# Kernel tuning notes

Hardware: AMD Instinct MI355X
Metric: run time of the kernel (lower is better)

Reference implementation:

```python
import jax, jax.numpy as jnp
import numpy as np

N, E = 50000, 800000
F_N, F_E = 32, 16
HC, H, C, L = 128, 2, 64, 3  # hidden_channels, heads, out per head, num_layers
NEG_SLOPE = 0.2  # PyG GATConv default


def setup_inputs() -> dict:
    key = jax.random.key(0)
    ks = jax.random.split(key, 32)
    rn = lambda k, shape, s=0.05: (jax.random.normal(k, shape, jnp.float32) * s)
    return {
        "x": jax.random.normal(ks[0], (N, F_N), jnp.float32),
        "edge_index": jax.random.randint(ks[1], (2, E), 0, N),
        "edge_attr": jax.random.normal(ks[2], (E, F_E), jnp.float32),
        # node encoder: Linear(32,128) -> ReLU -> Linear(128,128)
        "w_n1": rn(ks[3], (F_N, HC)), "b_n1": jnp.zeros((HC,), jnp.float32),
        "w_n2": rn(ks[4], (HC, HC)), "b_n2": jnp.zeros((HC,), jnp.float32),
        # edge encoder: Linear(16,128) -> ReLU (output is ignored by GATConv, edge_dim=None)
        "w_e": rn(ks[5], (F_E, HC)), "b_e": jnp.zeros((HC,), jnp.float32),
        # 3 GATConv layers: lin [128,H*C], att_src/att_dst [H,C], bias [H*C]
        "conv_w": rn(ks[6], (L, HC, H * C)),
        "conv_att_src": rn(ks[7], (L, H, C)),
        "conv_att_dst": rn(ks[8], (L, H, C)),
        "conv_b": jnp.zeros((L, H * C), jnp.float32),
        # path prediction head: Linear(256,128)->ReLU->Linear(128,64)->ReLU->Linear(64,1)->Sigmoid
        "wp1": rn(ks[9], (2 * HC, HC)), "bp1": jnp.zeros((HC,), jnp.float32),
        "wp2": rn(ks[10], (HC, 64)), "bp2": jnp.zeros((64,), jnp.float32),
        "wp3": rn(ks[11], (64, 1)), "bp3": jnp.zeros((1,), jnp.float32),
        # vulnerability head: Linear(128,64)->ReLU->Linear(64,1)->Sigmoid
        "wv1": rn(ks[12], (HC, 64)), "bv1": jnp.zeros((64,), jnp.float32),
        "wv2": rn(ks[13], (64, 1)), "bv2": jnp.zeros((1,), jnp.float32),
    }


def _gat_layer(x, src, dst, w, att_src, att_dst, bias):
    n = x.shape[0]
    h = (x @ w).reshape(n, H, C)                       # [N,H,C]
    a_src = jnp.sum(h * att_src, axis=-1)              # [N,H]
    a_dst = jnp.sum(h * att_dst, axis=-1)              # [N,H]
    alpha = a_src[src] + a_dst[dst]                    # [E',H]
    alpha = jax.nn.leaky_relu(alpha, NEG_SLOPE)
    amax = jax.lax.stop_gradient(jax.ops.segment_max(alpha, dst, num_segments=n))
    ex = jnp.exp(alpha - amax[dst])
    denom = jax.ops.segment_sum(ex, dst, num_segments=n)  # [N,H] (>0: self-loops)
    coef = ex / denom[dst]                             # softmax over incoming edges
    msg = h[src] * coef[:, :, None]                    # [E',H,C]
    out = jax.ops.segment_sum(msg, dst, num_segments=n)
    return out.reshape(n, H * C) + bias


def reference(x, edge_index, edge_attr,
              w_n1, b_n1, w_n2, b_n2, w_e, b_e,
              conv_w, conv_att_src, conv_att_dst, conv_b,
              wp1, bp1, wp2, bp2, wp3, bp3, wv1, bv1, wv2, bv2):
    n = x.shape[0]
    # node encoder (dropout = identity in eval)
    h = jax.nn.relu(x @ w_n1 + b_n1) @ w_n2 + b_n2
    # edge encoder output is computed but ignored by GATConv (edge_dim=None in PyG)
    _edge_emb = jax.nn.relu(edge_attr @ w_e + b_e)
    # add self loops (GATConv default add_self_loops=True)
    loop = jnp.arange(n, dtype=edge_index.dtype)
    src = jnp.concatenate([edge_index[0], loop])
    dst = jnp.concatenate([edge_index[1], loop])
    for l in range(L):
        h = jax.nn.relu(_gat_layer(h, src, dst, conv_w[l], conv_att_src[l], conv_att_dst[l], conv_b[l]))
    g = jnp.mean(h, axis=0, keepdims=True)             # [1,128] graph embedding
    # path head on cat(x[:1], graph_embedding)
    p = jnp.concatenate([h[:1], g], axis=1)            # [1,256]
    p = jax.nn.relu(p @ wp1 + bp1)
    p = jax.nn.relu(p @ wp2 + bp2)
    path = jax.nn.sigmoid(p @ wp3 + bp3)               # [1,1]
    v = jax.nn.relu(h @ wv1 + bv1)
    vuln = jax.nn.sigmoid(v @ wv2 + bv2)               # [N,1]
    esc = jnp.zeros((1, 1), jnp.float32)               # [1,1]
    return (path, vuln, esc)
```

## Files before the change

kernel.cpp:

```cpp
#include <hip/hip_runtime.h>
#include <math.h>

#define HC 128
#define NSLOPE 0.2f

__device__ __forceinline__ float lrelu(float v){ return v > 0.f ? v : NSLOPE * v; }

__device__ __forceinline__ unsigned short f2bf(float f){
    unsigned int b = __float_as_uint(f);
    b += 0x7FFFu + ((b >> 16) & 1u);
    return (unsigned short)(b >> 16);
}
__device__ __forceinline__ float bf_lo(unsigned int v){ return __uint_as_float(v << 16); }
__device__ __forceinline__ float bf_hi(unsigned int v){ return __uint_as_float(v & 0xFFFF0000u); }
__device__ __forceinline__ float bf1(unsigned short v){ return __uint_as_float((unsigned int)v << 16); }

__global__ void count_kernel(const int* __restrict__ ei, int* __restrict__ cnt,
                             int* __restrict__ rank, int E){
    int e = blockIdx.x * blockDim.x + threadIdx.x;
    if (e < E) rank[e] = atomicAdd(&cnt[ei[E + e]], 1);
}

__global__ __launch_bounds__(256) void scan_part_kernel(
        const int* __restrict__ deg, int* __restrict__ bsum, int n)
{
    int t = threadIdx.x, lane = t & 63, wid = t >> 6;
    int base = blockIdx.x * 1024 + t * 4;
    int s = 0;
    #pragma unroll
    for (int j = 0; j < 4; ++j){ int i = base + j; if (i < n) s += deg[i]; }
    #pragma unroll
    for (int o = 1; o < 64; o <<= 1) s += __shfl_xor(s, o);
    __shared__ int red[4];
    if (lane == 0) red[wid] = s;
    __syncthreads();
    if (t == 0) bsum[blockIdx.x] = red[0] + red[1] + red[2] + red[3];
}

__global__ __launch_bounds__(64) void scan_top_kernel(
        const int* __restrict__ bsum, int* __restrict__ boff, int* __restrict__ rowptr,
        int nb, int n)
{
    int t = threadIdx.x;
    int v = (t < nb) ? bsum[t] : 0;
    int incl = v;
    #pragma unroll
    for (int o = 1; o < 64; o <<= 1){ int u = __shfl_up(incl, o); if (t >= o) incl += u; }
    if (t < nb) boff[t] = incl - v;
    if (t == 63) rowptr[n] = incl;
}

__global__ __launch_bounds__(256) void scan_fin_kernel(
        const int* __restrict__ deg, const int* __restrict__ boff,
        int* __restrict__ rowptr, int n)
{
    int t = threadIdx.x, lane = t & 63, wid = t >> 6;
    int base = blockIdx.x * 1024 + t * 4;
    int d[4]; int s = 0;
    #pragma unroll
    for (int j = 0; j < 4; ++j){ int i = base + j; d[j] = (i < n) ? deg[i] : 0; s += d[j]; }
    int incl = s;
    #pragma unroll
    for (int o = 1; o < 64; o <<= 1){ int u = __shfl_up(incl, o); if (lane >= o) incl += u; }
    __shared__ int wsum[4];
    if (lane == 63) wsum[wid] = incl;
    __syncthreads();
    int off = boff[blockIdx.x] + (incl - s);
    for (int w = 0; w < wid; ++w) off += wsum[w];
    #pragma unroll
    for (int j = 0; j < 4; ++j){
        int i = base + j;
        if (i < n) rowptr[i] = off;
        off += d[j];
    }
}

__global__ __launch_bounds__(256) void scatter_kernel(
        const int* __restrict__ ei, const int* __restrict__ rowptr,
        const int* __restrict__ rank, int* __restrict__ colsrc, int E)
{
    int b = blockIdx.x * 1024 + threadIdx.x;
    int e0 = b, e1 = b + 256, e2 = b + 512, e3 = b + 768;
    bool v0 = e0 < E, v1 = e1 < E, v2 = e2 < E, v3 = e3 < E;
    int d0=0,d1=0,d2=0,d3=0, s0=0,s1=0,s2=0,s3=0, r0=0,r1=0,r2=0,r3=0;
    if (v0){ d0 = ei[E + e0]; s0 = ei[e0]; r0 = rank[e0]; }
    if (v1){ d1 = ei[E + e1]; s1 = ei[e1]; r1 = rank[e1]; }
    if (v2){ d2 = ei[E + e2]; s2 = ei[e2]; r2 = rank[e2]; }
    if (v3){ d3 = ei[E + e3]; s3 = ei[e3]; r3 = rank[e3]; }
    if (v0) colsrc[rowptr[d0] + r0] = s0;
    if (v1) colsrc[rowptr[d1] + r1] = s1;
    if (v2) colsrc[rowptr[d2] + r2] = s2;
    if (v3) colsrc[rowptr[d3] + r3] = s3;
}

__global__ __launch_bounds__(256) void enc1_kernel(
        const float* __restrict__ x, const float* __restrict__ w1, const float* __restrict__ b1,
        unsigned short* __restrict__ hid, int n)
{
    __shared__ float As[32][68];
    __shared__ float Bs[32][128];
    int t = threadIdx.x;
    int m0 = blockIdx.x * 64;
    int tm = t >> 4, tn = t & 15;

    #pragma unroll
    for (int i = 0; i < 2; ++i){
        int f = i * 256 + t;
        int row = f >> 3, kq = f & 7;
        int gr = m0 + row; if (gr > n - 1) gr = n - 1;
        float4 v = *(const float4*)(x + (size_t)gr * 32 + kq * 4);
        As[kq*4+0][row] = v.x; As[kq*4+1][row] = v.y; As[kq*4+2][row] = v.z; As[kq*4+3][row] = v.w;
    }
    #pragma unroll
    for (int i = 0; i < 4; ++i){
        int f = i * 256 + t;
        int kk = f >> 5, nq = f & 31;
        *(float4*)&Bs[kk][nq*4] = *(const float4*)(w1 + (size_t)kk * 128 + nq * 4);
    }
    __syncthreads();

    float acc[4][8];
    #pragma unroll
    for (int i = 0; i < 4; ++i)
        #pragma unroll
        for (int j = 0; j < 8; ++j) acc[i][j] = 0.f;

    #pragma unroll 4
    for (int k = 0; k < 32; ++k){
        float a[4], b[8];
        *(float4*)&a[0] = *(float4*)&As[k][tm*4];
        *(float4*)&b[0] = *(float4*)&Bs[k][tn*8];
        *(float4*)&b[4] = *(float4*)&Bs[k][tn*8+4];
        #pragma unroll
        for (int i = 0; i < 4; ++i)
            #pragma unroll
            for (int j = 0; j < 8; ++j) acc[i][j] = fmaf(a[i], b[j], acc[i][j]);
    }

    float bb[8];
    *(float4*)&bb[0] = *(const float4*)(b1 + tn*8);
    *(float4*)&bb[4] = *(const float4*)(b1 + tn*8 + 4);
    #pragma unroll
    for (int i = 0; i < 4; ++i){
        int node = m0 + tm*4 + i;
        if (node < n){
            float o[8];
            #pragma unroll
            for (int j = 0; j < 8; ++j) o[j] = fmaxf(acc[i][j] + bb[j], 0.f);
            uint4 pk;
            pk.x = (unsigned int)f2bf(o[0]) | ((unsigned int)f2bf(o[1]) << 16);
            pk.y = (unsigned int)f2bf(o[2]) | ((unsigned int)f2bf(o[3]) << 16);
            pk.z = (unsigned int)f2bf(o[4]) | ((unsigned int)f2bf(o[5]) << 16);
            pk.w = (unsigned int)f2bf(o[6]) | ((unsigned int)f2bf(o[7]) << 16);
            *(uint4*)(hid + (size_t)node*HC + tn*8) = pk;
        }
    }
}

template<bool ATT>
__global__ __launch_bounds__(256) void gemm_main_kernel(
        const unsigned short* __restrict__ A, const float* __restrict__ W, const float* __restrict__ bias,
        const float* __restrict__ att_s, const float* __restrict__ att_d,
        unsigned short* __restrict__ Cb,
        float* __restrict__ asrc, float* __restrict__ adst, int n)
{
    __shared__ float As[32][68];
    __shared__ float Bs[32][128];
    int t = threadIdx.x;
    int m0 = blockIdx.x * 64;
    int tm = t >> 4, tn = t & 15;

    float acc[4][8];
    #pragma unroll
    for (int i = 0; i < 4; ++i)
        #pragma unroll
        for (int j = 0; j < 8; ++j) acc[i][j] = 0.f;

    for (int kc = 0; kc < 4; ++kc){
        int k0 = kc * 32;
        {
            int row = t >> 2, kq = t & 3;
            int gr = m0 + row; if (gr > n - 1) gr = n - 1;
            uint4 v = *(const uint4*)(A + (size_t)gr * HC + k0 + kq * 8);
            As[kq*8+0][row] = bf_lo(v.x); As[kq*8+1][row] = bf_hi(v.x);
            As[kq*8+2][row] = bf_lo(v.y); As[kq*8+3][row] = bf_hi(v.y);
            As[kq*8+4][row] = bf_lo(v.z); As[kq*8+5][row] = bf_hi(v.z);
            As[kq*8+6][row] = bf_lo(v.w); As[kq*8+7][row] = bf_hi(v.w);
        }
        #pragma unroll
        for (int i = 0; i < 4; ++i){
            int f = i * 256 + t;
            int kk = f >> 5, nq = f & 31;
            *(float4*)&Bs[kk][nq*4] = *(const float4*)(W + (size_t)(k0 + kk) * 128 + nq * 4);
        }
        __syncthreads();
        #pragma unroll 4
        for (int k = 0; k < 32; ++k){
            float a[4], b[8];
            *(float4*)&a[0] = *(float4*)&As[k][tm*4];
            *(float4*)&b[0] = *(float4*)&Bs[k][tn*8];
            *(float4*)&b[4] = *(float4*)&Bs[k][tn*8+4];
            #pragma unroll
            for (int i = 0; i < 4; ++i)
                #pragma unroll
                for (int j = 0; j < 8; ++j) acc[i][j] = fmaf(a[i], b[j], acc[i][j]);
        }
        __syncthreads();
    }

    float bb[8];
    if (!ATT){
        *(float4*)&bb[0] = *(const float4*)(bias + tn*8);
        *(float4*)&bb[4] = *(const float4*)(bias + tn*8 + 4);
    } else {
        #pragma unroll
        for (int j = 0; j < 8; ++j) bb[j] = 0.f;
    }
    #pragma unroll
    for (int i = 0; i < 4; ++i){
        int node = m0 + tm*4 + i;
        if (node < n){
            float o[8];
            #pragma unroll
            for (int j = 0; j < 8; ++j) o[j] = acc[i][j] + bb[j];
            uint4 pk;
            pk.x = (unsigned int)f2bf(o[0]) | ((unsigned int)f2bf(o[1]) << 16);
            pk.y = (unsigned int)f2bf(o[2]) | ((unsigned int)f2bf(o[3]) << 16);
            pk.z = (unsigned int)f2bf(o[4]) | ((unsigned int)f2bf(o[5]) << 16);
            pk.w = (unsigned int)f2bf(o[6]) | ((unsigned int)f2bf(o[7]) << 16);
            *(uint4*)(Cb + (size_t)node*HC + tn*8) = pk;
        }
    }

    if (ATT){
        float ats[8], atd[8];
        *(float4*)&ats[0] = *(const float4*)(att_s + tn*8);
        *(float4*)&ats[4] = *(const float4*)(att_s + tn*8 + 4);
        *(float4*)&atd[0] = *(const float4*)(att_d + tn*8);
        *(float4*)&atd[4] = *(const float4*)(att_d + tn*8 + 4);
        #pragma unroll
        for (int i = 0; i < 4; ++i){
            float sa = 0.f, sd = 0.f;
            #pragma unroll
            for (int j = 0; j < 8; ++j){
                sa = fmaf(acc[i][j], ats[j], sa);
                sd = fmaf(acc[i][j], atd[j], sd);
            }
            sa += __shfl_xor(sa, 1); sa += __shfl_xor(sa, 2); sa += __shfl_xor(sa, 4);
            sd += __shfl_xor(sd, 1); sd += __shfl_xor(sd, 2); sd += __shfl_xor(sd, 4);
            int node = m0 + tm*4 + i;
            if ((tn == 0 || tn == 8) && node < n){
                int head = tn >> 3;
                asrc[(size_t)node*2 + head] = sa;
                adst[(size_t)node*2 + head] = sd;
            }
        }
    }
}

__global__ __launch_bounds__(64) void aggregate_kernel(
        const unsigned short* __restrict__ h1b, const float* __restrict__ asrc, const float* __restrict__ adst,
        const int* __restrict__ rowptr, const int* __restrict__ colsrc,
        const float* __restrict__ bias, unsigned short* __restrict__ hout, int n)
{
    __shared__ float4 exl[64];
    int i = blockIdx.x;
    if (i >= n) return;
    int t = threadIdx.x;
    int head = t >> 5;
    float2 adv = *(const float2*)(adst + (size_t)i * 2);
    float2 asv = *(const float2*)(asrc + (size_t)i * 2);
    float ads = head ? adv.y : adv.x;
    float exs = __expf(lrelu((head ? asv.y : asv.x) + ads));
    unsigned int hv = ((const unsigned int*)(h1b + (size_t)i * HC))[t];
    float acc0 = exs * bf_lo(hv), acc1 = exs * bf_hi(hv), D = exs;

    int e  = rowptr[i];
    int e1 = rowptr[i + 1];
    while (e < e1){
        int m = e1 - e; if (m > 64) m = 64;
        if (t < m){
            int s = colsrc[e + t];
            float2 as = *(const float2*)(asrc + (size_t)s * 2);
            exl[t] = make_float4(__int_as_float(s),
                                 __expf(lrelu(as.x + adv.x)),
                                 __expf(lrelu(as.y + adv.y)), 0.f);
        }
        __syncthreads();
        int j = 0;
        for (; j + 4 <= m; j += 4){
            float4 q0 = exl[j], q1 = exl[j+1], q2 = exl[j+2], q3 = exl[j+3];
            const unsigned int* p0 = (const unsigned int*)(h1b + (size_t)__float_as_int(q0.x) * HC);
            const unsigned int* p1 = (const unsigned int*)(h1b + (size_t)__float_as_int(q1.x) * HC);
            const unsigned int* p2 = (const unsigned int*)(h1b + (size_t)__float_as_int(q2.x) * HC);
            const unsigned int* p3 = (const unsigned int*)(h1b + (size_t)__float_as_int(q3.x) * HC);
            unsigned int v0 = p0[t], v1 = p1[t], v2 = p2[t], v3 = p3[t];
            float c0 = head ? q0.z : q0.y;
            float c1 = head ? q1.z : q1.y;
            float c2 = head ? q2.z : q2.y;
            float c3 = head ? q3.z : q3.y;
            acc0 = fmaf(c0, bf_lo(v0), acc0);  acc1 = fmaf(c0, bf_hi(v0), acc1);
            acc0 = fmaf(c1, bf_lo(v1), acc0);  acc1 = fmaf(c1, bf_hi(v1), acc1);
            acc0 = fmaf(c2, bf_lo(v2), acc0);  acc1 = fmaf(c2, bf_hi(v2), acc1);
            acc0 = fmaf(c3, bf_lo(v3), acc0);  acc1 = fmaf(c3, bf_hi(v3), acc1);
            D += (c0 + c1) + (c2 + c3);
        }
        for (; j < m; ++j){
            float4 q = exl[j];
            unsigned int v = ((const unsigned int*)(h1b + (size_t)__float_as_int(q.x) * HC))[t];
            float c = head ? q.z : q.y;
            acc0 = fmaf(c, bf_lo(v), acc0);
            acc1 = fmaf(c, bf_hi(v), acc1);
            D += c;
        }
        __syncthreads();
        e += m;
    }
    float rD = 1.0f / D;
    float o0 = fmaxf(acc0 * rD + bias[2*t],     0.f);
    float o1 = fmaxf(acc1 * rD + bias[2*t + 1], 0.f);
    ((unsigned int*)hout)[(size_t)i * 64 + t] =
        (unsigned int)f2bf(o0) | ((unsigned int)f2bf(o1) << 16);
}

__global__ __launch_bounds__(256) void mean_part_kernel(
        const unsigned short* __restrict__ h, float* __restrict__ partial, int n)
{
    int t = threadIdx.x;
    int cq = t & 31;
    int rl = t >> 5;
    float4 acc = make_float4(0.f, 0.f, 0.f, 0.f);
    for (int i = blockIdx.x * 8 + rl; i < n; i += gridDim.x * 8){
        uint2 v = *(const uint2*)(h + (size_t)i * HC + cq * 4);
        acc.x += bf_lo(v.x); acc.y += bf_hi(v.x);
        acc.z += bf_lo(v.y); acc.w += bf_hi(v.y);
    }
    __shared__ float4 red[256];
    red[t] = acc;
    __syncthreads();
    if (t < 128){
        float4 o = red[t + 128];
        red[t].x += o.x; red[t].y += o.y; red[t].z += o.z; red[t].w += o.w;
    }
    __syncthreads();
    if (t < 64){
        float4 o = red[t + 64];
        red[t].x += o.x; red[t].y += o.y; red[t].z += o.z; red[t].w += o.w;
    }
    __syncthreads();
    if (t < 32){
        float4 a = red[t], b = red[t + 32];
        float4 s = make_float4(a.x + b.x, a.y + b.y, a.z + b.z, a.w + b.w);
        *(float4*)(partial + (size_t)blockIdx.x * HC + t * 4) = s;
    }
}

__global__ __launch_bounds__(256) void mean_fin_kernel(
        const float* __restrict__ partial, float* __restrict__ g, int nb)
{
    int t = threadIdx.x;
    int cq = t & 31, b0 = t >> 5;
    float4 acc = make_float4(0.f, 0.f, 0.f, 0.f);
    for (int b = b0; b < nb; b += 8){
        float4 v = *(const float4*)(partial + (size_t)b * HC + cq * 4);
        acc.x += v.x; acc.y += v.y; acc.z += v.z; acc.w += v.w;
    }
    __shared__ float4 red[256];
    red[t] = acc;
    __syncthreads();
    if (t < 128){
        float4 o = red[t + 128];
        red[t].x += o.x; red[t].y += o.y; red[t].z += o.z; red[t].w += o.w;
    }
    __syncthreads();
    if (t < 64){
        float4 o = red[t + 64];
        red[t].x += o.x; red[t].y += o.y; red[t].z += o.z; red[t].w += o.w;
    }
    __syncthreads();
    if (t < 32){
        float4 a = red[t], b = red[t + 32];
        float4 s = make_float4(a.x + b.x, a.y + b.y, a.z + b.z, a.w + b.w);
        *(float4*)(g + t * 4) = s;
    }
}

__global__ __launch_bounds__(256) void vuln_fused_kernel(
        const unsigned short* __restrict__ h, const float* __restrict__ wv1, const float* __restrict__ bv1,
        const float* __restrict__ wv2, const float* __restrict__ bv2,
        float* __restrict__ out, int n)
{
    __shared__ float As[32][68];
    __shared__ float Bs[32][64];
    int t = threadIdx.x;
    int m0 = blockIdx.x * 64;
    int tm = t >> 4, tn = t & 15;

    float acc[4][4];
    #pragma unroll
    for (int i = 0; i < 4; ++i)
        #pragma unroll
        for (int j = 0; j < 4; ++j) acc[i][j] = 0.f;

    for (int kc = 0; kc < 4; ++kc){
        int k0 = kc * 32;
        {
            int row = t >> 2, kq = t & 3;
            int gr = m0 + row; if (gr > n - 1) gr = n - 1;
            uint4 v = *(const uint4*)(h + (size_t)gr * HC + k0 + kq * 8);
            As[kq*8+0][row] = bf_lo(v.x); As[kq*8+1][row] = bf_hi(v.x);
            As[kq*8+2][row] = bf_lo(v.y); As[kq*8+3][row] = bf_hi(v.y);
            As[kq*8+4][row] = bf_lo(v.z); As[kq*8+5][row] = bf_hi(v.z);
            As[kq*8+6][row] = bf_lo(v.w); As[kq*8+7][row] = bf_hi(v.w);
        }
        #pragma unroll
        for (int i = 0; i < 2; ++i){
            int f = i * 256 + t;
            int kk = f >> 4, nq = f & 15;
            *(float4*)&Bs[kk][nq*4] = *(const float4*)(wv1 + (size_t)(k0 + kk) * 64 + nq * 4);
        }
        __syncthreads();
        #pragma unroll 4
        for (int k = 0; k < 32; ++k){
            float a[4], b[4];
            *(float4*)&a[0] = *(float4*)&As[k][tm*4];
            *(float4*)&b[0] = *(float4*)&Bs[k][tn*4];
            #pragma unroll
            for (int i = 0; i < 4; ++i)
                #pragma unroll
                for (int j = 0; j < 4; ++j) acc[i][j] = fmaf(a[i], b[j], acc[i][j]);
        }
        __syncthreads();
    }

    float bb[4], wv[4];
    *(float4*)&bb[0] = *(const float4*)(bv1 + tn*4);
    *(float4*)&wv[0] = *(const float4*)(wv2 + tn*4);
    float bv2v = bv2[0];
    #pragma unroll
    for (int i = 0; i < 4; ++i){
        float v = 0.f;
        #pragma unroll
        for (int j = 0; j < 4; ++j) v = fmaf(fmaxf(acc[i][j] + bb[j], 0.f), wv[j], v);
        v += __shfl_xor(v, 1); v += __shfl_xor(v, 2);
        v += __shfl_xor(v, 4); v += __shfl_xor(v, 8);
        int node = m0 + tm*4 + i;
        if (tn == 0 && node < n)
            out[1 + node] = 1.0f / (1.0f + __expf(-(v + bv2v)));
    }
}

__global__ __launch_bounds__(128) void path_kernel(
        const unsigned short* __restrict__ h, const float* __restrict__ g,
        const float* __restrict__ wp1, const float* __restrict__ bp1,
        const float* __restrict__ wp2, const float* __restrict__ bp2,
        const float* __restrict__ wp3, const float* __restrict__ bp3,
        float* __restrict__ out, int n)
{
    __shared__ float pc[256];
    __shared__ float p1[HC];
    __shared__ float p2[64];
    int t = threadIdx.x;
    pc[t]       = bf1(h[t]);
    pc[128 + t] = g[t] * (1.0f / (float)n);
    __syncthreads();
    float a = bp1[t];
    for (int k = 0; k < 256; ++k) a = fmaf(pc[k], wp1[k * HC + t], a);
    p1[t] = fmaxf(a, 0.f);
    __syncthreads();
    if (t < 64){
        float a2 = bp2[t];
        for (int k = 0; k < HC; ++k) a2 = fmaf(p1[k], wp2[k * 64 + t], a2);
        p2[t] = fmaxf(a2, 0.f);
    }
    __syncthreads();
    if (t == 0){
        float a3 = bp3[0];
        for (int k = 0; k < 64; ++k) a3 = fmaf(p2[k], wp3[k], a3);
        out[0] = 1.0f / (1.0f + __expf(-a3));
        out[1 + n] = 0.f;
    }
}

extern "C" void kernel_launch(void* const* d_in, const int* in_sizes, int n_in,
                              void* d_out, int out_size, void* d_ws, size_t ws_size,
                              hipStream_t stream)
{
    const float* x    = (const float*)d_in[0];
    const int*   ei   = (const int*)d_in[1];
    const float* w_n1 = (const float*)d_in[3];
    const float* b_n1 = (const float*)d_in[4];
    const float* w_n2 = (const float*)d_in[5];
    const float* b_n2 = (const float*)d_in[6];
    const float* conv_w = (const float*)d_in[9];
    const float* att_s  = (const float*)d_in[10];
    const float* att_d  = (const float*)d_in[11];
    const float* conv_b = (const float*)d_in[12];
    const float* wp1 = (const float*)d_in[13];
    const float* bp1 = (const float*)d_in[14];
    const float* wp2 = (const float*)d_in[15];
    const float* bp2 = (const float*)d_in[16];
    const float* wp3 = (const float*)d_in[17];
    const float* bp3 = (const float*)d_in[18];
    const float* wv1 = (const float*)d_in[19];
    const float* bv1 = (const float*)d_in[20];
    const float* wv2 = (const float*)d_in[21];
    const float* bv2 = (const float*)d_in[22];

    const int N = in_sizes[0] / 32;
    const int E = in_sizes[1] / 2;
    float* out = (float*)d_out;

    char* ws = (char*)d_ws;
    size_t off = 0;
    auto take = [&](size_t bytes) -> char* {
        char* p = ws + off;
        off += (bytes + 255) & ~(size_t)255;
        return p;
    };
    unsigned short* hA = (unsigned short*)take((size_t)N * HC * 2);
    unsigned short* hB = (unsigned short*)take((size_t)N * HC * 2);
    float* asrc  = (float*)take((size_t)N * 2 * 4);
    float* adst  = (float*)take((size_t)N * 2 * 4);
    int*   rowptr= (int*)take((size_t)(N + 1) * 4);
    int*   cnt   = (int*)take((size_t)N * 4);
    int*   rank  = (int*)take((size_t)E * 4);
    int*   colsrc= (int*)take((size_t)E * 4);
    float* g     = (float*)take(HC * 4);
    const int MB = 64;
    float* mpart = (float*)take((size_t)MB * HC * 4);
    int nb = (N + 1023) / 1024;
    int*   bsum  = (int*)take((size_t)((nb + 63) & ~63) * 4);
    int*   boff  = (int*)take((size_t)((nb + 63) & ~63) * 4);

    hipMemsetAsync(cnt, 0, (size_t)N * 4, stream);
    count_kernel<<<(E + 255) / 256, 256, 0, stream>>>(ei, cnt, rank, E);
    scan_part_kernel<<<nb, 256, 0, stream>>>(cnt, bsum, N);
    scan_top_kernel<<<1, 64, 0, stream>>>(bsum, boff, rowptr, nb, N);
    scan_fin_kernel<<<nb, 256, 0, stream>>>(cnt, boff, rowptr, N);
    scatter_kernel<<<(E + 1023) / 1024, 256, 0, stream>>>(ei, rowptr, rank, colsrc, E);

    int nblk64 = (N + 63) / 64;
    enc1_kernel<<<nblk64, 256, 0, stream>>>(x, w_n1, b_n1, hB, N);
    gemm_main_kernel<false><<<nblk64, 256, 0, stream>>>(
        hB, w_n2, b_n2, nullptr, nullptr, hA, nullptr, nullptr, N);

    for (int l = 0; l < 3; ++l){
        gemm_main_kernel<true><<<nblk64, 256, 0, stream>>>(
            hA, conv_w + (size_t)l * HC * HC, nullptr,
            att_s + (size_t)l * HC, att_d + (size_t)l * HC,
            hB, asrc, adst, N);
        aggregate_kernel<<<N, 64, 0, stream>>>(
            hB, asrc, adst, rowptr, colsrc, conv_b + (size_t)l * HC, hA, N);
    }

    mean_part_kernel<<<MB, 256, 0, stream>>>(hA, mpart, N);
    mean_fin_kernel<<<1, 256, 0, stream>>>(mpart, g, MB);
    vuln_fused_kernel<<<nblk64, 256, 0, stream>>>(hA, wv1, bv1, wv2, bv2, out, N);
    path_kernel<<<1, 128, 0, stream>>>(hA, g, wp1, bp1, wp2, bp2, wp3, bp3, out, N);
}
```

Before: 372.5 us.

## Split GEMM over column halves and move attention dots to separate kernel

The main GEMM now runs twice as many blocks, each covering 64 output columns with a 4x4 per-thread tile and a smaller shared B tile, which should raise occupancy and parallelism. The attention-score dot products, which needed the full 128 columns in one block, move into a new att_kernel that rereads the bf16 projected features. The A-tile load mapping also changes so that consecutive threads cover consecutive rows (LDS write pattern), in both the main and vulnerability GEMMs. The cost is an extra launch per layer and an extra read of the projected features. Attention now uses bf16-rounded values rather than fp32 accumulators, a small precision change.

```diff
diff --git a/kernel.cpp b/kernel.cpp
--- a/kernel.cpp
+++ b/kernel.cpp
@@ -157,104 +157,101 @@
     }
 }
 
-template<bool ATT>
 __global__ __launch_bounds__(256) void gemm_main_kernel(
-        const unsigned short* __restrict__ A, const float* __restrict__ W, const float* __restrict__ bias,
-        const float* __restrict__ att_s, const float* __restrict__ att_d,
-        unsigned short* __restrict__ Cb,
-        float* __restrict__ asrc, float* __restrict__ adst, int n)
+        const unsigned short* __restrict__ A, const float* __restrict__ W,
+        const float* __restrict__ bias, unsigned short* __restrict__ Cb, int n)
 {
     __shared__ float As[32][68];
-    __shared__ float Bs[32][128];
-    int t = threadIdx.x;
-    int m0 = blockIdx.x * 64;
+    __shared__ float Bs[32][68];
+    int t = threadIdx.x;
+    int m0 = (blockIdx.x >> 1) * 64;
+    int c0 = (blockIdx.x & 1) * 64;
     int tm = t >> 4, tn = t & 15;
-
-    float acc[4][8];
+    int kq = t >> 6, arow = t & 63;
+
+    float acc[4][4];
     #pragma unroll
     for (int i = 0; i < 4; ++i)
         #pragma unroll
-        for (int j = 0; j < 8; ++j) acc[i][j] = 0.f;
+        for (int j = 0; j < 4; ++j) acc[i][j] = 0.f;
 
     for (int kc = 0; kc < 4; ++kc){
         int k0 = kc * 32;
         {
-            int row = t >> 2, kq = t & 3;
-            int gr = m0 + row; if (gr > n - 1) gr = n - 1;
+            int gr = m0 + arow; if (gr > n - 1) gr = n - 1;
             uint4 v = *(const uint4*)(A + (size_t)gr * HC + k0 + kq * 8);
-            As[kq*8+0][row] = bf_lo(v.x); As[kq*8+1][row] = bf_hi(v.x);
-            As[kq*8+2][row] = bf_lo(v.y); As[kq*8+3][row] = bf_hi(v.y);
-            As[kq*8+4][row] = bf_lo(v.z); As[kq*8+5][row] = bf_hi(v.z);
-            As[kq*8+6][row] = bf_lo(v.w); As[kq*8+7][row] = bf_hi(v.w);
-        }
-        #pragma unroll
-        for (int i = 0; i < 4; ++i){
+            As[kq*8+0][arow] = bf_lo(v.x); As[kq*8+1][arow] = bf_hi(v.x);
+            As[kq*8+2][arow] = bf_lo(v.y); As[kq*8+3][arow] = bf_hi(v.y);
+            As[kq*8+4][arow] = bf_lo(v.z); As[kq*8+5][arow] = bf_hi(v.z);
+            As[kq*8+6][arow] = bf_lo(v.w); As[kq*8+7][arow] = bf_hi(v.w);
+        }
+        #pragma unroll
+        for (int i = 0; i < 2; ++i){
             int f = i * 256 + t;
-            int kk = f >> 5, nq = f & 31;
-            *(float4*)&Bs[kk][nq*4] = *(const float4*)(W + (size_t)(k0 + kk) * 128 + nq * 4);
+            int kk = f >> 4, nq = f & 15;
+            *(float4*)&Bs[kk][nq*4] = *(const float4*)(W + (size_t)(k0 + kk) * 128 + c0 + nq * 4);
         }
         __syncthreads();
         #pragma unroll 4
         for (int k = 0; k < 32; ++k){
-            float a[4], b[8];
+            float a[4], b[4];
             *(float4*)&a[0] = *(float4*)&As[k][tm*4];
-            *(float4*)&b[0] = *(float4*)&Bs[k][tn*8];
-            *(float4*)&b[4] = *(float4*)&Bs[k][tn*8+4];
+            *(float4*)&b[0] = *(float4*)&Bs[k][tn*4];
             #pragma unroll
             for (int i = 0; i < 4; ++i)
                 #pragma unroll
-                for (int j = 0; j < 8; ++j) acc[i][j] = fmaf(a[i], b[j], acc[i][j]);
+                for (int j = 0; j < 4; ++j) acc[i][j] = fmaf(a[i], b[j], acc[i][j]);
         }
         __syncthreads();
     }
 
-    float bb[8];
-    if (!ATT){
-        *(float4*)&bb[0] = *(const float4*)(bias + tn*8);
-        *(float4*)&bb[4] = *(const float4*)(bias + tn*8 + 4);
+    float bb[4];
+    if (bias){
+        *(float4*)&bb[0] = *(const float4*)(bias + c0 + tn*4);
     } else {
         #pragma unroll
-        for (int j = 0; j < 8; ++j) bb[j] = 0.f;
+        for (int j = 0; j < 4; ++j) bb[j] = 0.f;
     }
     #pragma unroll
     for (int i = 0; i < 4; ++i){
         int node = m0 + tm*4 + i;
         if (node < n){
-            float o[8];
+            float o[4];
             #pragma unroll
-            for (int j = 0; j < 8; ++j) o[j] = acc[i][j] + bb[j];
-            uint4 pk;
+            for (int j = 0; j < 4; ++j) o[j] = acc[i][j] + bb[j];
+            uint2 pk;
             pk.x = (unsigned int)f2bf(o[0]) | ((unsigned int)f2bf(o[1]) << 16);
             pk.y = (unsigned int)f2bf(o[2]) | ((unsigned int)f2bf(o[3]) << 16);
-            pk.z = (unsigned int)f2bf(o[4]) | ((unsigned int)f2bf(o[5]) << 16);
-            pk.w = (unsigned int)f2bf(o[6]) | ((unsigned int)f2bf(o[7]) << 16);
-            *(uint4*)(Cb + (size_t)node*HC + tn*8) = pk;
-        }
-    }
-
-    if (ATT){
-        float ats[8], atd[8];
-        *(float4*)&ats[0] = *(const float4*)(att_s + tn*8);
-        *(float4*)&ats[4] = *(const float4*)(att_s + tn*8 + 4);
-        *(float4*)&atd[0] = *(const float4*)(att_d + tn*8);
-        *(float4*)&atd[4] = *(const float4*)(att_d + tn*8 + 4);
-        #pragma unroll
-        for (int i = 0; i < 4; ++i){
-            float sa = 0.f, sd = 0.f;
-            #pragma unroll
-            for (int j = 0; j < 8; ++j){
-                sa = fmaf(acc[i][j], ats[j], sa);
-                sd = fmaf(acc[i][j], atd[j], sd);
-            }
-            sa += __shfl_xor(sa, 1); sa += __shfl_xor(sa, 2); sa += __shfl_xor(sa, 4);
-            sd += __shfl_xor(sd, 1); sd += __shfl_xor(sd, 2); sd += __shfl_xor(sd, 4);
-            int node = m0 + tm*4 + i;
-            if ((tn == 0 || tn == 8) && node < n){
-                int head = tn >> 3;
-                asrc[(size_t)node*2 + head] = sa;
-                adst[(size_t)node*2 + head] = sd;
-            }
-        }
+            *(uint2*)(Cb + (size_t)node*HC + c0 + tn*4) = pk;
+        }
+    }
+}
+
+__global__ __launch_bounds__(256) void att_kernel(
+        const unsigned short* __restrict__ h1, const float* __restrict__ att_s,
+        const float* __restrict__ att_d, float* __restrict__ asrc, float* __restrict__ adst, int n)
+{
+    int t = threadIdx.x;
+    int node = blockIdx.x * 32 + (t >> 3);
+    int l8 = t & 7;
+    if (node >= n) return;
+    uint4 v0 = *(const uint4*)(h1 + (size_t)node * HC + l8 * 16);
+    uint4 v1 = *(const uint4*)(h1 + (size_t)node * HC + l8 * 16 + 8);
+    float sa = 0.f, sd = 0.f;
+    unsigned int w[8] = {v0.x, v0.y, v0.z, v0.w, v1.x, v1.y, v1.z, v1.w};
+    #pragma unroll
+    for (int q = 0; q < 8; ++q){
+        float lo = bf_lo(w[q]), hi = bf_hi(w[q]);
+        int c = l8 * 16 + q * 2;
+        sa = fmaf(lo, att_s[c], sa);     sa = fmaf(hi, att_s[c + 1], sa);
+        sd = fmaf(lo, att_d[c], sd);     sd = fmaf(hi, att_d[c + 1], sd);
+    }
+    sa += __shfl_xor(sa, 1); sa += __shfl_xor(sa, 2);
+    sd += __shfl_xor(sd, 1); sd += __shfl_xor(sd, 2);
+    if ((l8 & 3) == 0){
+        int head = l8 >> 2;
+        asrc[(size_t)node * 2 + head] = sa;
+        adst[(size_t)node * 2 + head] = sd;
     }
 }
 
@@ -395,6 +392,7 @@
     int t = threadIdx.x;
     int m0 = blockIdx.x * 64;
     int tm = t >> 4, tn = t & 15;
+    int kq = t >> 6, arow = t & 63;
 
     float acc[4][4];
     #pragma unroll
@@ -405,13 +403,12 @@
     for (int kc = 0; kc < 4; ++kc){
         int k0 = kc * 32;
         {
-            int row = t >> 2, kq = t & 3;
-            int gr = m0 + row; if (gr > n - 1) gr = n - 1;
+            int gr = m0 + arow; if (gr > n - 1) gr = n - 1;
             uint4 v = *(const uint4*)(h + (size_t)gr * HC + k0 + kq * 8);
-            As[kq*8+0][row] = bf_lo(v.x); As[kq*8+1][row] = bf_hi(v.x);
-            As[kq*8+2][row] = bf_lo(v.y); As[kq*8+3][row] = bf_hi(v.y);
-            As[kq*8+4][row] = bf_lo(v.z); As[kq*8+5][row] = bf_hi(v.z);
-            As[kq*8+6][row] = bf_lo(v.w); As[kq*8+7][row] = bf_hi(v.w);
+            As[kq*8+0][arow] = bf_lo(v.x); As[kq*8+1][arow] = bf_hi(v.x);
+            As[kq*8+2][arow] = bf_lo(v.y); As[kq*8+3][arow] = bf_hi(v.y);
+            As[kq*8+4][arow] = bf_lo(v.z); As[kq*8+5][arow] = bf_hi(v.z);
+            As[kq*8+6][arow] = bf_lo(v.w); As[kq*8+7][arow] = bf_hi(v.w);
         }
         #pragma unroll
         for (int i = 0; i < 2; ++i){
@@ -541,15 +538,15 @@
     scatter_kernel<<<(E + 1023) / 1024, 256, 0, stream>>>(ei, rowptr, rank, colsrc, E);
 
     int nblk64 = (N + 63) / 64;
+    int gemm_grid = nblk64 * 2;
     enc1_kernel<<<nblk64, 256, 0, stream>>>(x, w_n1, b_n1, hB, N);
-    gemm_main_kernel<false><<<nblk64, 256, 0, stream>>>(
-        hB, w_n2, b_n2, nullptr, nullptr, hA, nullptr, nullptr, N);
+    gemm_main_kernel<<<gemm_grid, 256, 0, stream>>>(hB, w_n2, b_n2, hA, N);
 
     for (int l = 0; l < 3; ++l){
-        gemm_main_kernel<true><<<nblk64, 256, 0, stream>>>(
-            hA, conv_w + (size_t)l * HC * HC, nullptr,
-            att_s + (size_t)l * HC, att_d + (size_t)l * HC,
-            hB, asrc, adst, N);
+        gemm_main_kernel<<<gemm_grid, 256, 0, stream>>>(
+            hA, conv_w + (size_t)l * HC * HC, nullptr, hB, N);
+        att_kernel<<<(N + 31) / 32, 256, 0, stream>>>(
+            hB, att_s + (size_t)l * HC, att_d + (size_t)l * HC, asrc, adst, N);
         aggregate_kernel<<<N, 64, 0, stream>>>(
             hB, asrc, adst, rowptr, colsrc, conv_b + (size_t)l * HC, hA, N);
     }
```

Result: no change. 366.0 us (-1.7%).

## Use bf16 MFMA for node encoder and GAT linear GEMMs with pre-transposed weights

Applied to the files above, without the earlier changes.

Replaces the scalar-FMA LDS-tiled 128x128 GEMM with a per-wave 16x16x32 bf16 MFMA kernel that reads A rows and a pre-transposed bf16 weight directly from global memory. A small kernel converts and transposes the weights to bf16 each call. The attention dot products are computed from the MFMA accumulators with shuffle reductions, and outputs are restaged through LDS for coalesced bf16 stores. Weights now lose precision to bf16, and the vuln kernel's A-tile load indexing is also remapped.

```diff
diff --git a/kernel.cpp b/kernel.cpp
--- a/kernel.cpp
+++ b/kernel.cpp
@@ -3,6 +3,9 @@
 
 #define HC 128
 #define NSLOPE 0.2f
+
+using bf16x8 = __attribute__((ext_vector_type(8))) short;
+using f32x4  = __attribute__((ext_vector_type(4))) float;
 
 __device__ __forceinline__ float lrelu(float v){ return v > 0.f ? v : NSLOPE * v; }
 
@@ -93,6 +96,26 @@
     if (v3) colsrc[rowptr[d3] + r3] = s3;
 }
 
+__global__ __launch_bounds__(256) void wtrans_kernel(
+        const float* __restrict__ W, unsigned short* __restrict__ Wt, int nmat)
+{
+    int idx = blockIdx.x * 256 + threadIdx.x;
+    if (idx >= nmat * 2048) return;
+    int mat = idx >> 11;
+    int rem = idx & 2047;
+    int c = rem >> 4, kg = rem & 15;
+    const float* Wm = W + (size_t)mat * 16384;
+    unsigned short* Wo = Wt + (size_t)mat * 16384;
+    unsigned int pk[4];
+    #pragma unroll
+    for (int j = 0; j < 4; ++j){
+        float a = Wm[(size_t)(kg*8 + j*2    ) * 128 + c];
+        float b = Wm[(size_t)(kg*8 + j*2 + 1) * 128 + c];
+        pk[j] = (unsigned int)f2bf(a) | ((unsigned int)f2bf(b) << 16);
+    }
+    *(uint4*)(Wo + (size_t)c * 128 + kg * 8) = make_uint4(pk[0], pk[1], pk[2], pk[3]);
+}
+
 __global__ __launch_bounds__(256) void enc1_kernel(
         const float* __restrict__ x, const float* __restrict__ w1, const float* __restrict__ b1,
         unsigned short* __restrict__ hid, int n)
@@ -158,102 +181,96 @@
 }
 
 template<bool ATT>
-__global__ __launch_bounds__(256) void gemm_main_kernel(
-        const unsigned short* __restrict__ A, const float* __restrict__ W, const float* __restrict__ bias,
+__global__ __launch_bounds__(256) void gemm_mfma_kernel(
+        const unsigned short* __restrict__ A, const unsigned short* __restrict__ Wt,
+        const float* __restrict__ bias,
         const float* __restrict__ att_s, const float* __restrict__ att_d,
         unsigned short* __restrict__ Cb,
         float* __restrict__ asrc, float* __restrict__ adst, int n)
 {
-    __shared__ float As[32][68];
-    __shared__ float Bs[32][128];
-    int t = threadIdx.x;
-    int m0 = blockIdx.x * 64;
-    int tm = t >> 4, tn = t & 15;
-
-    float acc[4][8];
-    #pragma unroll
-    for (int i = 0; i < 4; ++i)
-        #pragma unroll
-        for (int j = 0; j < 8; ++j) acc[i][j] = 0.f;
-
+    __shared__ float lds[4][16][132];
+    int t = threadIdx.x;
+    int w = t >> 6, l = t & 63;
+    int lane15 = l & 15, lanehi = l >> 4;
+    int m0 = blockIdx.x * 64 + w * 16;
+
+    f32x4 acc[8];
+    #pragma unroll
+    for (int ct = 0; ct < 8; ++ct) acc[ct] = (f32x4){0.f, 0.f, 0.f, 0.f};
+
+    int ar = m0 + lane15; if (ar > n - 1) ar = n - 1;
+    const unsigned short* Arow = A + (size_t)ar * HC;
+
+    #pragma unroll
     for (int kc = 0; kc < 4; ++kc){
-        int k0 = kc * 32;
-        {
-            int row = t >> 2, kq = t & 3;
-            int gr = m0 + row; if (gr > n - 1) gr = n - 1;
-            uint4 v = *(const uint4*)(A + (size_t)gr * HC + k0 + kq * 8);
-            As[kq*8+0][row] = bf_lo(v.x); As[kq*8+1][row] = bf_hi(v.x);
-            As[kq*8+2][row] = bf_lo(v.y); As[kq*8+3][row] = bf_hi(v.y);
-            As[kq*8+4][row] = bf_lo(v.z); As[kq*8+5][row] = bf_hi(v.z);
-            As[kq*8+6][row] = bf_lo(v.w); As[kq*8+7][row] = bf_hi(v.w);
-        }
-        #pragma unroll
-        for (int i = 0; i < 4; ++i){
-            int f = i * 256 + t;
-            int kk = f >> 5, nq = f & 31;
-            *(float4*)&Bs[kk][nq*4] = *(const float4*)(W + (size_t)(k0 + kk) * 128 + nq * 4);
-        }
-        __syncthreads();
-        #pragma unroll 4
-        for (int k = 0; k < 32; ++k){
-            float a[4], b[8];
-            *(float4*)&a[0] = *(float4*)&As[k][tm*4];
-            *(float4*)&b[0] = *(float4*)&Bs[k][tn*8];
-            *(float4*)&b[4] = *(float4*)&Bs[k][tn*8+4];
+        bf16x8 af = *reinterpret_cast<const bf16x8*>(Arow + kc * 32 + lanehi * 8);
+        #pragma unroll
+        for (int ct = 0; ct < 8; ++ct){
+            bf16x8 bf = *reinterpret_cast<const bf16x8*>(
+                Wt + (size_t)(ct * 16 + lane15) * HC + kc * 32 + lanehi * 8);
+            acc[ct] = __builtin_amdgcn_mfma_f32_16x16x32_bf16(af, bf, acc[ct], 0, 0, 0);
+        }
+    }
+
+    if (ATT){
+        float ats[8], atd[8];
+        #pragma unroll
+        for (int ct = 0; ct < 8; ++ct){
+            ats[ct] = att_s[ct * 16 + lane15];
+            atd[ct] = att_d[ct * 16 + lane15];
+        }
+        #pragma unroll
+        for (int r = 0; r < 4; ++r){
+            float sa0 = 0.f, sd0 = 0.f, sa1 = 0.f, sd1 = 0.f;
             #pragma unroll
-            for (int i = 0; i < 4; ++i)
-                #pragma unroll
-                for (int j = 0; j < 8; ++j) acc[i][j] = fmaf(a[i], b[j], acc[i][j]);
-        }
-        __syncthreads();
+            for (int ct = 0; ct < 4; ++ct){
+                sa0 = fmaf(acc[ct][r], ats[ct], sa0);
+                sd0 = fmaf(acc[ct][r], atd[ct], sd0);
+            }
+            #pragma unroll
+            for (int ct = 4; ct < 8; ++ct){
+                sa1 = fmaf(acc[ct][r], ats[ct], sa1);
+                sd1 = fmaf(acc[ct][r], atd[ct], sd1);
+            }
+            #pragma unroll
+            for (int o = 1; o < 16; o <<= 1){
+                sa0 += __shfl_xor(sa0, o); sd0 += __shfl_xor(sd0, o);
+                sa1 += __shfl_xor(sa1, o); sd1 += __shfl_xor(sd1, o);
+            }
+            int node = m0 + lanehi * 4 + r;
+            if (lane15 == 0 && node < n){
+                asrc[(size_t)node * 2]     = sa0;
+                adst[(size_t)node * 2]     = sd0;
+                asrc[(size_t)node * 2 + 1] = sa1;
+                adst[(size_t)node * 2 + 1] = sd1;
+            }
+        }
     }
 
     float bb[8];
-    if (!ATT){
-        *(float4*)&bb[0] = *(const float4*)(bias + tn*8);
-        *(float4*)&bb[4] = *(const float4*)(bias + tn*8 + 4);
-    } else {
-        #pragma unroll
-        for (int j = 0; j < 8; ++j) bb[j] = 0.f;
-    }
-    #pragma unroll
-    for (int i = 0; i < 4; ++i){
-        int node = m0 + tm*4 + i;
-        if (node < n){
+    #pragma unroll
+    for (int ct = 0; ct < 8; ++ct) bb[ct] = ATT ? 0.f : bias[ct * 16 + lane15];
+    #pragma unroll
+    for (int ct = 0; ct < 8; ++ct)
+        #pragma unroll
+        for (int r = 0; r < 4; ++r)
+            lds[w][lanehi * 4 + r][ct * 16 + lane15] = acc[ct][r] + bb[ct];
+    __syncthreads();
+
+    int row = lane15, cb = lanehi;
+    int node = m0 + row;
+    if (node < n){
+        #pragma unroll
+        for (int q = 0; q < 4; ++q){
             float o[8];
-            #pragma unroll
-            for (int j = 0; j < 8; ++j) o[j] = acc[i][j] + bb[j];
+            *(float4*)&o[0] = *(float4*)&lds[w][row][cb * 32 + q * 8];
+            *(float4*)&o[4] = *(float4*)&lds[w][row][cb * 32 + q * 8 + 4];
             uint4 pk;
             pk.x = (unsigned int)f2bf(o[0]) | ((unsigned int)f2bf(o[1]) << 16);
             pk.y = (unsigned int)f2bf(o[2]) | ((unsigned int)f2bf(o[3]) << 16);
             pk.z = (unsigned int)f2bf(o[4]) | ((unsigned int)f2bf(o[5]) << 16);
             pk.w = (unsigned int)f2bf(o[6]) | ((unsigned int)f2bf(o[7]) << 16);
-            *(uint4*)(Cb + (size_t)node*HC + tn*8) = pk;
-        }
-    }
-
-    if (ATT){
-        float ats[8], atd[8];
-        *(float4*)&ats[0] = *(const float4*)(att_s + tn*8);
-        *(float4*)&ats[4] = *(const float4*)(att_s + tn*8 + 4);
-        *(float4*)&atd[0] = *(const float4*)(att_d + tn*8);
-        *(float4*)&atd[4] = *(const float4*)(att_d + tn*8 + 4);
-        #pragma unroll
-        for (int i = 0; i < 4; ++i){
-            float sa = 0.f, sd = 0.f;
-            #pragma unroll
-            for (int j = 0; j < 8; ++j){
-                sa = fmaf(acc[i][j], ats[j], sa);
-                sd = fmaf(acc[i][j], atd[j], sd);
-            }
-            sa += __shfl_xor(sa, 1); sa += __shfl_xor(sa, 2); sa += __shfl_xor(sa, 4);
-            sd += __shfl_xor(sd, 1); sd += __shfl_xor(sd, 2); sd += __shfl_xor(sd, 4);
-            int node = m0 + tm*4 + i;
-            if ((tn == 0 || tn == 8) && node < n){
-                int head = tn >> 3;
-                asrc[(size_t)node*2 + head] = sa;
-                adst[(size_t)node*2 + head] = sd;
-            }
+            *(uint4*)(Cb + (size_t)node * HC + cb * 32 + q * 8) = pk;
         }
     }
 }
@@ -395,6 +412,7 @@
     int t = threadIdx.x;
     int m0 = blockIdx.x * 64;
     int tm = t >> 4, tn = t & 15;
+    int kq = t >> 6, arow = t & 63;
 
     float acc[4][4];
     #pragma unroll
@@ -405,13 +423,12 @@
     for (int kc = 0; kc < 4; ++kc){
         int k0 = kc * 32;
         {
-            int row = t >> 2, kq = t & 3;
-            int gr = m0 + row; if (gr > n - 1) gr = n - 1;
+            int gr = m0 + arow; if (gr > n - 1) gr = n - 1;
             uint4 v = *(const uint4*)(h + (size_t)gr * HC + k0 + kq * 8);
-            As[kq*8+0][row] = bf_lo(v.x); As[kq*8+1][row] = bf_hi(v.x);
-            As[kq*8+2][row] = bf_lo(v.y); As[kq*8+3][row] = bf_hi(v.y);
-            As[kq*8+4][row] = bf_lo(v.z); As[kq*8+5][row] = bf_hi(v.z);
-            As[kq*8+6][row] = bf_lo(v.w); As[kq*8+7][row] = bf_hi(v.w);
+            As[kq*8+0][arow] = bf_lo(v.x); As[kq*8+1][arow] = bf_hi(v.x);
+            As[kq*8+2][arow] = bf_lo(v.y); As[kq*8+3][arow] = bf_hi(v.y);
+            As[kq*8+4][arow] = bf_lo(v.z); As[kq*8+5][arow] = bf_hi(v.z);
+            As[kq*8+6][arow] = bf_lo(v.w); As[kq*8+7][arow] = bf_hi(v.w);
         }
         #pragma unroll
         for (int i = 0; i < 2; ++i){
@@ -527,6 +544,8 @@
     int*   rank  = (int*)take((size_t)E * 4);
     int*   colsrc= (int*)take((size_t)E * 4);
     float* g     = (float*)take(HC * 4);
+    unsigned short* Wt0 = (unsigned short*)take(16384 * 2);
+    unsigned short* Wt1 = (unsigned short*)take((size_t)3 * 16384 * 2);
     const int MB = 64;
     float* mpart = (float*)take((size_t)MB * HC * 4);
     int nb = (N + 1023) / 1024;
@@ -540,14 +559,17 @@
     scan_fin_kernel<<<nb, 256, 0, stream>>>(cnt, boff, rowptr, N);
     scatter_kernel<<<(E + 1023) / 1024, 256, 0, stream>>>(ei, rowptr, rank, colsrc, E);
 
+    wtrans_kernel<<<8, 256, 0, stream>>>(w_n2, Wt0, 1);
+    wtrans_kernel<<<24, 256, 0, stream>>>(conv_w, Wt1, 3);
+
     int nblk64 = (N + 63) / 64;
     enc1_kernel<<<nblk64, 256, 0, stream>>>(x, w_n1, b_n1, hB, N);
-    gemm_main_kernel<false><<<nblk64, 256, 0, stream>>>(
-        hB, w_n2, b_n2, nullptr, nullptr, hA, nullptr, nullptr, N);
+    gemm_mfma_kernel<false><<<nblk64, 256, 0, stream>>>(
+        hB, Wt0, b_n2, nullptr, nullptr, hA, nullptr, nullptr, N);
 
     for (int l = 0; l < 3; ++l){
-        gemm_main_kernel<true><<<nblk64, 256, 0, stream>>>(
-            hA, conv_w + (size_t)l * HC * HC, nullptr,
+        gemm_mfma_kernel<true><<<nblk64, 256, 0, stream>>>(
+            hA, Wt1 + (size_t)l * 16384, nullptr,
             att_s + (size_t)l * HC, att_d + (size_t)l * HC,
             hB, asrc, adst, N);
         aggregate_kernel<<<N, 64, 0, stream>>>(
```

After: 336.8 us. 1.11x faster.
